# Performance work log

Hardware: AMD Instinct MI355X
Metric: run time of the kernel (lower is better)

## Reference

```python
import jax, jax.numpy as jnp
import numpy as np

CURV = 1.0          # manifold curvature c
HEADS = 4
HEAD_DIM = 32       # (dim-1) // heads = 128 // 4
SCALE = HEAD_DIM ** -0.5
EPS = 1e-7

N_NODES = 50000
N_EDGES = 800000
D = 128             # tangent feature dim (dim - 1)


def log_origin(x, c):
    """Lorentz log map at the origin o=(1/sqrt(c),0,...); returns spatial (d) part of tangent."""
    sc = jnp.sqrt(c)
    x0 = x[..., 0]
    xs = x[..., 1:]
    norm = jnp.sqrt(jnp.sum(xs * xs, axis=-1) + EPS)         # (N,)
    dist = jnp.arccosh(jnp.maximum(sc * x0, 1.0 + EPS)) / sc  # (N,)
    return (dist / norm)[..., None] * xs                      # (N, d)


def exp_origin(vs, c):
    """Lorentz exp map at origin of tangent vector (0, vs); returns point (N, d+1)."""
    sc = jnp.sqrt(c)
    r = jnp.sqrt(jnp.sum(vs * vs, axis=-1) + EPS)  # (N,)
    arg = sc * r
    x0 = jnp.cosh(arg) / sc
    xs = (jnp.sinh(arg) / arg)[..., None] * vs
    return jnp.concatenate([x0[..., None], xs], axis=-1)


def setup_inputs() -> dict:
    key = jax.random.key(0)
    k1, k2, k3, k4, k5, k6, k7 = jax.random.split(key, 7)
    # valid hyperboloid points: x0 = sqrt(1/c + ||xs||^2)
    xs = 0.5 * jax.random.normal(k1, (N_NODES, D), dtype=jnp.float32)
    x0 = jnp.sqrt(1.0 / CURV + jnp.sum(xs * xs, axis=-1, keepdims=True))
    x = jnp.concatenate([x0, xs], axis=-1)  # (N, d+1)
    edge_index = jax.random.randint(k2, (2, N_EDGES), 0, N_NODES, dtype=jnp.int64)
    s = D ** -0.5
    Wq = s * jax.random.normal(k3, (D, D), dtype=jnp.float32)
    Wk = s * jax.random.normal(k4, (D, D), dtype=jnp.float32)
    Wv = s * jax.random.normal(k5, (D, D), dtype=jnp.float32)
    Wo = s * jax.random.normal(k6, (D, D), dtype=jnp.float32)
    bo = jnp.zeros((D,), dtype=jnp.float32)
    return {"x": x, "edge_index": edge_index, "Wq": Wq, "Wk": Wk, "Wv": Wv, "Wo": Wo, "bo": bo}


def reference(x, edge_index, Wq, Wk, Wv, Wo, bo):
    N = x.shape[0]
    row, col = edge_index[0], edge_index[1]
    # map to tangent space at origin, drop the (zero) time component
    x_tan = log_origin(x, CURV)                       # (N, d)
    Q = (x_tan @ Wq.T).reshape(N, HEADS, HEAD_DIM)
    K = (x_tan @ Wk.T).reshape(N, HEADS, HEAD_DIM)
    V = (x_tan @ Wv.T).reshape(N, HEADS, HEAD_DIM)
    # per-edge attention logits, grouped softmax over incoming edges of each target node (col)
    scores = jnp.einsum('ehd,ehd->eh', Q[col], K[row]) * SCALE   # (E, H)
    m = jax.ops.segment_max(scores, col, num_segments=N)         # (N, H)
    e = jnp.exp(scores - m[col])
    denom = jax.ops.segment_sum(e, col, num_segments=N)          # (N, H)
    att = e / denom[col]                                         # (E, H)
    # weighted scatter-sum of values
    agg = jax.ops.segment_sum(att[..., None] * V[row], col, num_segments=N)  # (N, H, hd)
    agg = agg.reshape(N, HEADS * HEAD_DIM)
    out = agg @ Wo.T + bo                                        # (N, d)
    # lift back: prepend zero time component, exp map at origin
    return exp_origin(out, CURV)                                 # (N, d+1)
```

## Files before the change

### kernel.cpp

```cpp
#include <hip/hip_runtime.h>
#include <hip/hip_fp8.h>
#include <math.h>

#define EPS 1e-7f
#define SCALE 0.17677669529663687f
#define MAXDEG 64

typedef _Float16 half2v __attribute__((ext_vector_type(2)));
typedef _Float16 f16x4 __attribute__((ext_vector_type(4)));
typedef _Float16 f16x8 __attribute__((ext_vector_type(8)));
typedef float f32x4 __attribute__((ext_vector_type(4)));

__device__ __forceinline__ void gload16(const void* g, void* l) {
  __builtin_amdgcn_global_load_lds(
      (const __attribute__((address_space(1))) unsigned int*)g,
      (__attribute__((address_space(3))) unsigned int*)l, 16, 0, 0);
}

__device__ __forceinline__ float f8tof(unsigned char u) {
  __hip_fp8_e4m3 h;
  h.__x = (__hip_fp8_storage_t)u;
  return (float)h;
}
__device__ __forceinline__ unsigned char ftof8(float f) {
  __hip_fp8_e4m3 h(f);
  return (unsigned char)h.__x;
}

__global__ __launch_bounds__(256) void prep_kernel(
    const float* __restrict__ x,
    const float* __restrict__ Wq, const float* __restrict__ Wk,
    const float* __restrict__ Wv, const float* __restrict__ Wo,
    _Float16* __restrict__ Wc, _Float16* __restrict__ Wof,
    _Float16* __restrict__ xt, int* __restrict__ cnt, int N) {
  int b = blockIdx.x;
  if (b < 256) {
    int o = b * 256 + threadIdx.x;
    int j = o >> 7;
    int i = o & 127;
    if (j < 384) {
      const float* W = (j < 128) ? Wq : (j < 256) ? Wk : Wv;
      Wc[o] = (_Float16)W[(j & 127) * 128 + i];
    } else {
      Wof[(j - 384) * 128 + i] = (_Float16)Wo[(j - 384) * 128 + i];
    }
    return;
  }
  int node = (b - 256) * 4 + (threadIdx.x >> 6);
  if (node >= N) return;
  int lane = threadIdx.x & 63;
  float2 xs = *reinterpret_cast<const float2*>(&x[(size_t)node * 129 + 1 + lane * 2]);
  float ss = fmaf(xs.x, xs.x, xs.y * xs.y);
#pragma unroll
  for (int o = 32; o >= 1; o >>= 1) ss += __shfl_xor(ss, o, 64);
  float norm = sqrtf(ss + EPS);
  float x0 = x[(size_t)node * 129];
  float dist = acoshf(fmaxf(x0, 1.0f + EPS));
  float sc = dist / norm;
  half2v h;
  h.x = (_Float16)(sc * xs.x);
  h.y = (_Float16)(sc * xs.y);
  *reinterpret_cast<half2v*>(&xt[(size_t)node * 128 + lane * 2]) = h;
  if (lane == 0) cnt[node] = 0;
}

template <int NCHUNKS, int MODE>
__global__ __launch_bounds__(256, 3) void gemm_mfma(
    const _Float16* __restrict__ A,
    const _Float16* __restrict__ B,
    void* __restrict__ C0, void* __restrict__ C1,
    const float* __restrict__ bias, int M,
    const int* __restrict__ col, const int* __restrict__ row,
    int* __restrict__ cnt, int* __restrict__ rml, int E) {
  int bid;
  if (MODE == 0) {
    if ((blockIdx.x & 1) == 0) {
      int stride = (gridDim.x >> 1) * 256;
      for (int e = (blockIdx.x >> 1) * 256 + threadIdx.x; e < E; e += stride) {
        int c = col[e];
        int pos = atomicAdd(&cnt[c], 1);
        if (pos < MAXDEG) rml[c * MAXDEG + pos] = row[e];
      }
      return;
    }
    bid = blockIdx.x >> 1;
  } else {
    bid = blockIdx.x;
  }

  __shared__ _Float16 As[64 * 128];
  __shared__ _Float16 Bs[128 * 128];
  const int tid = threadIdx.x;
  const int wave = tid >> 6;
  const int lane = tid & 63;
  const int wm = wave >> 1, wn = wave & 1;
  const int lrow = lane & 15, q = lane >> 4;
  const int m0 = bid * 64;

#pragma unroll
  for (int j = 0; j < 4; j++) {
    int slot0 = (j * 4 + wave) * 64;
    int p = slot0 + lane;
    int m = p >> 4;
    int kcl = (p & 15) ^ (m & 15);
    int msrc = m0 + m;
    if (msrc > M - 1) msrc = M - 1;
    gload16(A + (size_t)msrc * 128 + kcl * 8, (char*)As + (size_t)slot0 * 16);
  }

  f32x4 acc[2][4];
  for (int c = 0; c < NCHUNKS; c++) {
#pragma unroll
    for (int j = 0; j < 8; j++) {
      int slot0 = (j * 4 + wave) * 64;
      int p = slot0 + lane;
      int n = p >> 4;
      int kcl = (p & 15) ^ (n & 15);
      gload16(B + ((size_t)(c * 128 + n)) * 128 + kcl * 8, (char*)Bs + (size_t)slot0 * 16);
    }
    __syncthreads();

#pragma unroll
    for (int mt = 0; mt < 2; mt++)
#pragma unroll
      for (int nt = 0; nt < 4; nt++) acc[mt][nt] = (f32x4)0.f;

    const f16x8* Av = (const f16x8*)As;
    const f16x8* Bv = (const f16x8*)Bs;
#pragma unroll
    for (int s = 0; s < 4; s++) {
      int kc = s * 4 + q;
      f16x8 af[2], bf[4];
#pragma unroll
      for (int mt = 0; mt < 2; mt++) {
        int m = wm * 32 + mt * 16 + lrow;
        af[mt] = Av[m * 16 + (kc ^ (m & 15))];
      }
#pragma unroll
      for (int nt = 0; nt < 4; nt++) {
        int n = wn * 64 + nt * 16 + lrow;
        bf[nt] = Bv[n * 16 + (kc ^ (n & 15))];
      }
#pragma unroll
      for (int mt = 0; mt < 2; mt++)
#pragma unroll
        for (int nt = 0; nt < 4; nt++)
          acc[mt][nt] = __builtin_amdgcn_mfma_f32_16x16x32_f16(af[mt], bf[nt], acc[mt][nt], 0, 0, 0);
    }

    if (MODE == 0) {
#pragma unroll
      for (int mt = 0; mt < 2; mt++) {
#pragma unroll
        for (int reg = 0; reg < 4; reg++) {
          int rg = m0 + wm * 32 + mt * 16 + q * 4 + reg;
          if (rg < M) {
#pragma unroll
            for (int nt = 0; nt < 4; nt++) {
              int cl = wn * 64 + nt * 16 + lrow;
              float v = acc[mt][nt][reg];
              if (c == 0) {
                ((_Float16*)C0)[(size_t)rg * 128 + cl] = (_Float16)v;
              } else {
                int h = cl >> 5, j = cl & 31;
                int idx = (h * 8 + (j >> 2)) * 8 + ((c == 2) ? 4 : 0) + (j & 3);
                ((unsigned char*)C1)[(size_t)rg * 256 + idx] = ftof8(v);
              }
            }
          }
        }
      }
      if (c + 1 < NCHUNKS) __syncthreads();
    }
  }

  if (MODE == 1) {
    float* out = (float*)C0;
    __syncthreads();
    float* rsum = (float*)As;
#pragma unroll
    for (int mt = 0; mt < 2; mt++)
#pragma unroll
      for (int nt = 0; nt < 4; nt++) {
        int cl = wn * 64 + nt * 16 + lrow;
        float b = bias[cl];
#pragma unroll
        for (int reg = 0; reg < 4; reg++) acc[mt][nt][reg] += b;
      }
#pragma unroll
    for (int mt = 0; mt < 2; mt++) {
#pragma unroll
      for (int reg = 0; reg < 4; reg++) {
        float s4 = 0.f;
#pragma unroll
        for (int nt = 0; nt < 4; nt++) s4 = fmaf(acc[mt][nt][reg], acc[mt][nt][reg], s4);
#pragma unroll
        for (int o = 8; o >= 1; o >>= 1) s4 += __shfl_xor(s4, o, 16);
        if (lrow == 0) rsum[(wm * 32 + mt * 16 + q * 4 + reg) * 2 + wn] = s4;
      }
    }
    __syncthreads();
#pragma unroll
    for (int mt = 0; mt < 2; mt++) {
#pragma unroll
      for (int reg = 0; reg < 4; reg++) {
        int rl = wm * 32 + mt * 16 + q * 4 + reg;
        int rg = m0 + rl;
        if (rg < M) {
          float tot = rsum[rl * 2] + rsum[rl * 2 + 1];
          float r = sqrtf(tot + EPS);
          float s = sinhf(r) / r;
#pragma unroll
          for (int nt = 0; nt < 4; nt++) {
            int cl = wn * 64 + nt * 16 + lrow;
            out[(size_t)rg * 129 + 1 + cl] = s * acc[mt][nt][reg];
          }
          if (wn == 0 && lrow == 0) out[(size_t)rg * 129] = coshf(r);
        }
      }
    }
  }
}

__global__ __launch_bounds__(256) void attn_kernel(
    const _Float16* __restrict__ Qb,
    const unsigned char* __restrict__ KVI,
    const int* __restrict__ rml, const int* __restrict__ cnt,
    _Float16* __restrict__ agg, int N) {
  int node = blockIdx.x * 4 + (threadIdx.x >> 6);
  if (node >= N) return;
  int lane = threadIdx.x & 63;
  int par = lane >> 5;
  int hd = lane & 31;
  int qoff = hd * 4;
  f16x4 qh = *reinterpret_cast<const f16x4*>(Qb + (size_t)node * 128 + qoff);
  float q0 = (float)qh[0], q1 = (float)qh[1], q2 = (float)qh[2], q3 = (float)qh[3];
  int deg = cnt[node];
  if (deg > MAXDEG) deg = MAXDEG;
  const int* el = rml + (size_t)node * MAXDEG;
  float l = 0.f, av0 = 0.f, av1 = 0.f, av2 = 0.f, av3 = 0.f;

  auto dot = [&](uint2 w, float& p, float& v0, float& v1, float& v2, float& v3) {
    unsigned kx = w.x, vx = w.y;
    float k0 = f8tof(kx & 255), k1 = f8tof((kx >> 8) & 255);
    float k2 = f8tof((kx >> 16) & 255), k3 = f8tof(kx >> 24);
    v0 = f8tof(vx & 255); v1 = f8tof((vx >> 8) & 255);
    v2 = f8tof((vx >> 16) & 255); v3 = f8tof(vx >> 24);
    p = fmaf(q0, k0, fmaf(q1, k1, fmaf(q2, k2, q3 * k3)));
  };

  int i = 0;
  for (; i + 8 <= deg; i += 8) {
    int rA = el[i + par], rB = el[i + 2 + par], rC = el[i + 4 + par], rD = el[i + 6 + par];
    uint2 wA = *reinterpret_cast<const uint2*>(KVI + (size_t)rA * 256 + hd * 8);
    uint2 wB = *reinterpret_cast<const uint2*>(KVI + (size_t)rB * 256 + hd * 8);
    uint2 wC = *reinterpret_cast<const uint2*>(KVI + (size_t)rC * 256 + hd * 8);
    uint2 wD = *reinterpret_cast<const uint2*>(KVI + (size_t)rD * 256 + hd * 8);
    float pA, a4, a5, a6, a7;
    float pB, b4, b5, b6, b7;
    float pC, c4, c5, c6, c7;
    float pD, d4, d5, d6, d7;
    dot(wA, pA, a4, a5, a6, a7);
    dot(wB, pB, b4, b5, b6, b7);
    dot(wC, pC, c4, c5, c6, c7);
    dot(wD, pD, d4, d5, d6, d7);
#pragma unroll
    for (int o = 4; o >= 1; o >>= 1) {
      pA += __shfl_xor(pA, o, 8);
      pB += __shfl_xor(pB, o, 8);
      pC += __shfl_xor(pC, o, 8);
      pD += __shfl_xor(pD, o, 8);
    }
    float eA = __expf(pA * SCALE);
    float eB = __expf(pB * SCALE);
    float eC = __expf(pC * SCALE);
    float eD = __expf(pD * SCALE);
    l += (eA + eB) + (eC + eD);
    av0 = fmaf(eA, a4, av0); av0 = fmaf(eB, b4, av0);
    av1 = fmaf(eA, a5, av1); av1 = fmaf(eB, b5, av1);
    av2 = fmaf(eA, a6, av2); av2 = fmaf(eB, b6, av2);
    av3 = fmaf(eA, a7, av3); av3 = fmaf(eB, b7, av3);
    av0 = fmaf(eC, c4, av0); av0 = fmaf(eD, d4, av0);
    av1 = fmaf(eC, c5, av1); av1 = fmaf(eD, d5, av1);
    av2 = fmaf(eC, c6, av2); av2 = fmaf(eD, d6, av2);
    av3 = fmaf(eC, c7, av3); av3 = fmaf(eD, d7, av3);
  }
  for (; i + 2 <= deg; i += 2) {
    int rA = el[i + par];
    uint2 wA = *reinterpret_cast<const uint2*>(KVI + (size_t)rA * 256 + hd * 8);
    float pA, a4, a5, a6, a7;
    dot(wA, pA, a4, a5, a6, a7);
#pragma unroll
    for (int o = 4; o >= 1; o >>= 1) pA += __shfl_xor(pA, o, 8);
    float eA = __expf(pA * SCALE);
    l += eA;
    av0 = fmaf(eA, a4, av0);
    av1 = fmaf(eA, a5, av1);
    av2 = fmaf(eA, a6, av2);
    av3 = fmaf(eA, a7, av3);
  }
  if (i < deg) {
    int r = el[i];
    uint2 wA = *reinterpret_cast<const uint2*>(KVI + (size_t)r * 256 + hd * 8);
    float pA, a4, a5, a6, a7;
    dot(wA, pA, a4, a5, a6, a7);
#pragma unroll
    for (int o = 4; o >= 1; o >>= 1) pA += __shfl_xor(pA, o, 8);
    float e = __expf(pA * SCALE) * (par ? 0.f : 1.f);
    l += e;
    av0 = fmaf(e, a4, av0);
    av1 = fmaf(e, a5, av1);
    av2 = fmaf(e, a6, av2);
    av3 = fmaf(e, a7, av3);
  }
  l += __shfl_xor(l, 32, 64);
  av0 += __shfl_xor(av0, 32, 64);
  av1 += __shfl_xor(av1, 32, 64);
  av2 += __shfl_xor(av2, 32, 64);
  av3 += __shfl_xor(av3, 32, 64);
  if (par == 0) {
    float inv = (l > 0.f) ? 1.0f / l : 0.f;
    f16x4 o4;
    o4[0] = (_Float16)(av0 * inv);
    o4[1] = (_Float16)(av1 * inv);
    o4[2] = (_Float16)(av2 * inv);
    o4[3] = (_Float16)(av3 * inv);
    *reinterpret_cast<f16x4*>(agg + (size_t)node * 128 + qoff) = o4;
  }
}

extern "C" void kernel_launch(void* const* d_in, const int* in_sizes, int n_in,
                              void* d_out, int out_size, void* d_ws, size_t ws_size,
                              hipStream_t stream) {
  const float* x = (const float*)d_in[0];
  const int* ei = (const int*)d_in[1];
  const float* Wq = (const float*)d_in[2];
  const float* Wk = (const float*)d_in[3];
  const float* Wv = (const float*)d_in[4];
  const float* Wo = (const float*)d_in[5];
  const float* bo = (const float*)d_in[6];
  float* out = (float*)d_out;

  const int N = in_sizes[0] / 129;
  const int E = in_sizes[1] / 2;
  const int* row = ei;
  const int* col = ei + E;

  char* ws = (char*)d_ws;
  size_t off = 0;
  auto alloc = [&](size_t bytes) -> void* {
    off = (off + 255) & ~(size_t)255;
    void* p = ws + off;
    off += bytes;
    return p;
  };
  _Float16* xtan = (_Float16*)alloc((size_t)N * 128 * 2);
  _Float16* qbuf = (_Float16*)alloc((size_t)N * 128 * 2);
  unsigned char* kvi = (unsigned char*)alloc((size_t)N * 256);
  int* rml       = (int*)alloc((size_t)N * MAXDEG * 4);
  _Float16* Wc   = (_Float16*)alloc(384 * 128 * 2);
  _Float16* Wof  = (_Float16*)alloc(128 * 128 * 2);
  int* cnt       = (int*)alloc((size_t)(N + 1) * 4);

  const int gemm_nb = (N + 63) / 64;

  prep_kernel<<<256 + (N + 3) / 4, 256, 0, stream>>>(x, Wq, Wk, Wv, Wo, Wc, Wof,
                                                     xtan, cnt, N);
  gemm_mfma<3, 0><<<gemm_nb * 2, 256, 0, stream>>>(xtan, Wc, qbuf, kvi, nullptr, N,
                                                   col, row, cnt, rml, E);
  attn_kernel<<<(N + 3) / 4, 256, 0, stream>>>(qbuf, kvi, rml, cnt, xtan, N);
  gemm_mfma<1, 1><<<gemm_nb, 256, 0, stream>>>(xtan, Wof, out, nullptr, bo, N,
                                               nullptr, nullptr, nullptr, nullptr, 0);
}
```

Baseline: 196.9 us.

## Fuse Lorentz log map into QKV GEMM A-tile load and restructure edge scatter

The log-origin map moves out of the prep kernel and into the QKV GEMM. Each block reads fp32 x rows directly, computes norm and acosh scale per row with a 4-lane shuffle, and writes swizzled fp16 tiles straight into LDS. This removes the fp16 x_tan round trip through global memory, and the prep kernel now only converts weights and zeroes counters. The edge-bucketing blocks change from an interleaved grid-stride loop to one edge per thread in a dedicated leading block range, and attention output goes to a separate buffer. The A-tile load now goes through registers instead of the async global-to-LDS path, and the counter zeroing relies on N fitting in 65536 threads.

```diff
diff --git a/kernel.cpp b/kernel.cpp
--- a/kernel.cpp
+++ b/kernel.cpp
@@ -28,62 +28,43 @@
 }
 
 __global__ __launch_bounds__(256) void prep_kernel(
-    const float* __restrict__ x,
     const float* __restrict__ Wq, const float* __restrict__ Wk,
     const float* __restrict__ Wv, const float* __restrict__ Wo,
     _Float16* __restrict__ Wc, _Float16* __restrict__ Wof,
-    _Float16* __restrict__ xt, int* __restrict__ cnt, int N) {
-  int b = blockIdx.x;
-  if (b < 256) {
-    int o = b * 256 + threadIdx.x;
-    int j = o >> 7;
-    int i = o & 127;
-    if (j < 384) {
-      const float* W = (j < 128) ? Wq : (j < 256) ? Wk : Wv;
-      Wc[o] = (_Float16)W[(j & 127) * 128 + i];
-    } else {
-      Wof[(j - 384) * 128 + i] = (_Float16)Wo[(j - 384) * 128 + i];
-    }
-    return;
-  }
-  int node = (b - 256) * 4 + (threadIdx.x >> 6);
-  if (node >= N) return;
-  int lane = threadIdx.x & 63;
-  float2 xs = *reinterpret_cast<const float2*>(&x[(size_t)node * 129 + 1 + lane * 2]);
-  float ss = fmaf(xs.x, xs.x, xs.y * xs.y);
-#pragma unroll
-  for (int o = 32; o >= 1; o >>= 1) ss += __shfl_xor(ss, o, 64);
-  float norm = sqrtf(ss + EPS);
-  float x0 = x[(size_t)node * 129];
-  float dist = acoshf(fmaxf(x0, 1.0f + EPS));
-  float sc = dist / norm;
-  half2v h;
-  h.x = (_Float16)(sc * xs.x);
-  h.y = (_Float16)(sc * xs.y);
-  *reinterpret_cast<half2v*>(&xt[(size_t)node * 128 + lane * 2]) = h;
-  if (lane == 0) cnt[node] = 0;
+    int* __restrict__ cnt, int N) {
+  int o = blockIdx.x * 256 + threadIdx.x;
+  int j = o >> 7;
+  int i = o & 127;
+  if (j < 384) {
+    const float* W = (j < 128) ? Wq : (j < 256) ? Wk : Wv;
+    Wc[o] = (_Float16)W[(j & 127) * 128 + i];
+  } else {
+    Wof[(j - 384) * 128 + i] = (_Float16)Wo[(j - 384) * 128 + i];
+  }
+  if (o <= N) cnt[o] = 0;
 }
 
 template <int NCHUNKS, int MODE>
 __global__ __launch_bounds__(256, 3) void gemm_mfma(
+    const float* __restrict__ X,
     const _Float16* __restrict__ A,
     const _Float16* __restrict__ B,
     void* __restrict__ C0, void* __restrict__ C1,
     const float* __restrict__ bias, int M,
     const int* __restrict__ col, const int* __restrict__ row,
-    int* __restrict__ cnt, int* __restrict__ rml, int E) {
+    int* __restrict__ cnt, int* __restrict__ rml, int E, int SB) {
   int bid;
   if (MODE == 0) {
-    if ((blockIdx.x & 1) == 0) {
-      int stride = (gridDim.x >> 1) * 256;
-      for (int e = (blockIdx.x >> 1) * 256 + threadIdx.x; e < E; e += stride) {
+    if ((int)blockIdx.x < SB) {
+      int e = blockIdx.x * 256 + threadIdx.x;
+      if (e < E) {
         int c = col[e];
         int pos = atomicAdd(&cnt[c], 1);
         if (pos < MAXDEG) rml[c * MAXDEG + pos] = row[e];
       }
       return;
     }
-    bid = blockIdx.x >> 1;
+    bid = blockIdx.x - SB;
   } else {
     bid = blockIdx.x;
   }
@@ -97,15 +78,46 @@
   const int lrow = lane & 15, q = lane >> 4;
   const int m0 = bid * 64;
 
-#pragma unroll
-  for (int j = 0; j < 4; j++) {
-    int slot0 = (j * 4 + wave) * 64;
-    int p = slot0 + lane;
-    int m = p >> 4;
-    int kcl = (p & 15) ^ (m & 15);
+  if (MODE == 0) {
+    int m = tid >> 2, qd = tid & 3;
     int msrc = m0 + m;
     if (msrc > M - 1) msrc = M - 1;
-    gload16(A + (size_t)msrc * 128 + kcl * 8, (char*)As + (size_t)slot0 * 16);
+    const float* xr = X + (size_t)msrc * 129;
+    float4 f4[8];
+    float ss = 0.f;
+#pragma unroll
+    for (int j = 0; j < 8; j++) {
+      f4[j] = *reinterpret_cast<const float4*>(xr + 1 + qd * 32 + j * 4);
+      ss = fmaf(f4[j].x, f4[j].x, fmaf(f4[j].y, f4[j].y,
+           fmaf(f4[j].z, f4[j].z, fmaf(f4[j].w, f4[j].w, ss))));
+    }
+    ss += __shfl_xor(ss, 1, 4);
+    ss += __shfl_xor(ss, 2, 4);
+    float x0 = xr[0];
+    float dist = acoshf(fmaxf(x0, 1.0f + EPS));
+    float sc = dist / sqrtf(ss + EPS);
+#pragma unroll
+    for (int j = 0; j < 4; j++) {
+      float4 a = f4[j * 2], b = f4[j * 2 + 1];
+      f16x8 ch;
+      ch[0] = (_Float16)(sc * a.x); ch[1] = (_Float16)(sc * a.y);
+      ch[2] = (_Float16)(sc * a.z); ch[3] = (_Float16)(sc * a.w);
+      ch[4] = (_Float16)(sc * b.x); ch[5] = (_Float16)(sc * b.y);
+      ch[6] = (_Float16)(sc * b.z); ch[7] = (_Float16)(sc * b.w);
+      int kc = qd * 4 + j;
+      ((f16x8*)As)[m * 16 + (kc ^ (m & 15))] = ch;
+    }
+  } else {
+#pragma unroll
+    for (int j = 0; j < 4; j++) {
+      int slot0 = (j * 4 + wave) * 64;
+      int p = slot0 + lane;
+      int m = p >> 4;
+      int kcl = (p & 15) ^ (m & 15);
+      int msrc = m0 + m;
+      if (msrc > M - 1) msrc = M - 1;
+      gload16(A + (size_t)msrc * 128 + kcl * 8, (char*)As + (size_t)slot0 * 16);
+    }
   }
 
   f32x4 acc[2][4];
@@ -354,8 +366,8 @@
     off += bytes;
     return p;
   };
-  _Float16* xtan = (_Float16*)alloc((size_t)N * 128 * 2);
   _Float16* qbuf = (_Float16*)alloc((size_t)N * 128 * 2);
+  _Float16* agg  = (_Float16*)alloc((size_t)N * 128 * 2);
   unsigned char* kvi = (unsigned char*)alloc((size_t)N * 256);
   int* rml       = (int*)alloc((size_t)N * MAXDEG * 4);
   _Float16* Wc   = (_Float16*)alloc(384 * 128 * 2);
@@ -363,12 +375,14 @@
   int* cnt       = (int*)alloc((size_t)(N + 1) * 4);
 
   const int gemm_nb = (N + 63) / 64;
-
-  prep_kernel<<<256 + (N + 3) / 4, 256, 0, stream>>>(x, Wq, Wk, Wv, Wo, Wc, Wof,
-                                                     xtan, cnt, N);
-  gemm_mfma<3, 0><<<gemm_nb * 2, 256, 0, stream>>>(xtan, Wc, qbuf, kvi, nullptr, N,
-                                                   col, row, cnt, rml, E);
-  attn_kernel<<<(N + 3) / 4, 256, 0, stream>>>(qbuf, kvi, rml, cnt, xtan, N);
-  gemm_mfma<1, 1><<<gemm_nb, 256, 0, stream>>>(xtan, Wof, out, nullptr, bo, N,
-                                               nullptr, nullptr, nullptr, nullptr, 0);
-}
+  const int SB = (E + 255) / 256;
+
+  prep_kernel<<<256, 256, 0, stream>>>(Wq, Wk, Wv, Wo, Wc, Wof, cnt, N);
+  gemm_mfma<3, 0><<<SB + gemm_nb, 256, 0, stream>>>(x, nullptr, Wc, qbuf, kvi,
+                                                    nullptr, N, col, row, cnt,
+                                                    rml, E, SB);
+  attn_kernel<<<(N + 3) / 4, 256, 0, stream>>>(qbuf, kvi, rml, cnt, agg, N);
+  gemm_mfma<1, 1><<<gemm_nb, 256, 0, stream>>>(nullptr, agg, Wof, out, nullptr,
+                                               bo, N, nullptr, nullptr, nullptr,
+                                               nullptr, 0, 0);
+}
```

Measured after the change: 234.8 us. 19.2% more time.
